# Optimization experiments

Measured on AMD Instinct MI355X. Metric: run time of the kernel, lower is better.

## Reference

```python
import jax, jax.numpy as jnp
import numpy as np

N, M, D = 8192, 8192, 1024

def setup_inputs() -> dict:
    key = jax.random.key(0)
    k1, k2 = jax.random.split(key)
    encoder_outputs = jax.random.normal(k1, (N, D), dtype=jnp.float32)
    fact_emb = jax.random.normal(k2, (M, D), dtype=jnp.float32)
    return {"encoder_outputs": encoder_outputs, "fact_emb": fact_emb}

def reference(encoder_outputs, fact_emb):
    # energy: [N, M] = encoder_outputs @ fact_emb^T (unscaled)
    energy = jnp.einsum('nd,md->nm', encoder_outputs, fact_emb)
    weights = jax.nn.softmax(energy, axis=1)          # softmax over facts
    outputs = jnp.einsum('nm,md->nd', weights, fact_emb)
    return (outputs, weights)
```

## Files before the change

kernel.cpp:

```cpp
#include <hip/hip_runtime.h>
#include <hip/hip_bf16.h>
#include <math.h>
#include <stdint.h>

#define N_ROWS 8192
#define M_FACTS 8192
#define D_DIM 1024

typedef __bf16 bf16x8_t __attribute__((ext_vector_type(8)));
typedef __bf16 bf16x4_t __attribute__((ext_vector_type(4)));
typedef float f32x4_t __attribute__((ext_vector_type(4)));

#define BM 128
#define BN 128
#define BK 32
#define PADK 40

__device__ __forceinline__ void gload_lds16(const void* g, void* lds) {
  __builtin_amdgcn_global_load_lds(
      (__attribute__((address_space(1))) void*)(uintptr_t)g,
      (__attribute__((address_space(3))) void*)(uint32_t)(uintptr_t)lds,
      16, 0, 0);
}


__global__ __launch_bounds__(256) void split_hi_lo(const float* __restrict__ X,
                                                   __bf16* __restrict__ H,
                                                   __bf16* __restrict__ L) {
  int i = blockIdx.x * 256 + threadIdx.x;
  float4 v = ((const float4*)X)[i];
  float f[4] = {v.x, v.y, v.z, v.w};
  bf16x4_t h, l;
#pragma unroll
  for (int q = 0; q < 4; q++) {
    __bf16 hh = (__bf16)f[q];
    h[q] = hh;
    l[q] = (__bf16)(f[q] - (float)hh);
  }
  ((bf16x4_t*)H)[i] = h;
  ((bf16x4_t*)L)[i] = l;
}

__global__ __launch_bounds__(256) void transpose_f_bf16(const float* __restrict__ F,
                                                        __bf16* __restrict__ Ft) {
  __shared__ __bf16 t[64 * 68];
  const int tid = threadIdx.x;
  const int m0 = blockIdx.x * 64, d0 = blockIdx.y * 64;
#pragma unroll
  for (int p = 0; p < 4; p++) {
    int flat = p * 256 + tid;
    int m = flat >> 4, dq = flat & 15;
    float4 v = *(const float4*)(F + (size_t)(m0 + m) * D_DIM + d0 + dq * 4);
    bf16x4_t h;
    h[0] = (__bf16)v.x;
    h[1] = (__bf16)v.y;
    h[2] = (__bf16)v.z;
    h[3] = (__bf16)v.w;
    *(bf16x4_t*)(t + m * 68 + dq * 4) = h;
  }
  __syncthreads();
  int d = tid & 63, mc = (tid >> 6) * 16;
  bf16x8_t o0, o1;
#pragma unroll
  for (int j = 0; j < 8; j++) o0[j] = t[(mc + j) * 68 + d];
#pragma unroll
  for (int j = 0; j < 8; j++) o1[j] = t[(mc + 8 + j) * 68 + d];
  __bf16* dst = Ft + (size_t)(d0 + d) * M_FACTS + m0 + mc;
  *(bf16x8_t*)(dst) = o0;
  *(bf16x8_t*)(dst + 8) = o1;
}

__global__ __launch_bounds__(256) void gemm1_fast(const __bf16* __restrict__ Eh,
                                                  const __bf16* __restrict__ El,
                                                  const __bf16* __restrict__ Fh,
                                                  const __bf16* __restrict__ Fl,
                                                  float* __restrict__ C) {
  __shared__ __bf16 sAh[BM * BK], sAl[BM * BK], sBh[BN * BK], sBl[BN * BK];
  const int tid = threadIdx.x;
  const int wave = tid >> 6, lane = tid & 63;
  const int row0 = blockIdx.x * BM, col0 = blockIdx.y * BN;
  const int wm = wave >> 1, wn = wave & 1;
  const int lrow = lane & 15, quad = lane >> 4;

  f32x4_t acc[4][4];
#pragma unroll
  for (int i = 0; i < 4; i++)
#pragma unroll
    for (int j = 0; j < 4; j++) acc[i][j] = (f32x4_t){0.f, 0.f, 0.f, 0.f};

  for (int k0 = 0; k0 < D_DIM; k0 += BK) {
#pragma unroll
    for (int r = 0; r < 2; r++) {
      int c = (r * 4 + wave) * 64 + lane;
      int row = c >> 2;
      int ko = (c & 3) << 3;
      size_t ga = (size_t)(row0 + row) * D_DIM + k0 + ko;
      size_t gb = (size_t)(col0 + row) * D_DIM + k0 + ko;
      gload_lds16(Eh + ga, sAh + c * 8);
      gload_lds16(El + ga, sAl + c * 8);
      gload_lds16(Fh + gb, sBh + c * 8);
      gload_lds16(Fl + gb, sBl + c * 8);
    }
    __syncthreads();

    bf16x8_t ah[4], al[4], bh[4], bl[4];
#pragma unroll
    for (int i = 0; i < 4; i++) {
      int ra = (wm * 64 + i * 16 + lrow) * BK + quad * 8;
      ah[i] = *(const bf16x8_t*)(sAh + ra);
      al[i] = *(const bf16x8_t*)(sAl + ra);
      int rb = (wn * 64 + i * 16 + lrow) * BK + quad * 8;
      bh[i] = *(const bf16x8_t*)(sBh + rb);
      bl[i] = *(const bf16x8_t*)(sBl + rb);
    }
#pragma unroll
    for (int i = 0; i < 4; i++)
#pragma unroll
      for (int j = 0; j < 4; j++) {
        acc[i][j] = __builtin_amdgcn_mfma_f32_16x16x32_bf16(ah[i], bh[j], acc[i][j], 0, 0, 0);
        acc[i][j] = __builtin_amdgcn_mfma_f32_16x16x32_bf16(ah[i], bl[j], acc[i][j], 0, 0, 0);
        acc[i][j] = __builtin_amdgcn_mfma_f32_16x16x32_bf16(al[i], bh[j], acc[i][j], 0, 0, 0);
      }
    __syncthreads();
  }

#pragma unroll
  for (int i = 0; i < 4; i++) {
    int rbase = row0 + wm * 64 + i * 16 + quad * 4;
#pragma unroll
    for (int j = 0; j < 4; j++) {
      int c = col0 + wn * 64 + j * 16 + lrow;
#pragma unroll
      for (int r = 0; r < 4; r++) C[(size_t)(rbase + r) * M_FACTS + c] = acc[i][j][r];
    }
  }
}

__global__ __launch_bounds__(256) void gemm2_fast(const __bf16* __restrict__ Wb,
                                                  const __bf16* __restrict__ Ft,
                                                  float* __restrict__ O,
                                                  int out_row0) {
  __shared__ __bf16 sW[BM * BK], sF[BN * BK];
  const int tid = threadIdx.x;
  const int wave = tid >> 6, lane = tid & 63;
  const int row0 = blockIdx.x * BM, col0 = blockIdx.y * BN;
  const int wm = wave >> 1, wn = wave & 1;
  const int lrow = lane & 15, quad = lane >> 4;

  f32x4_t acc[4][4];
#pragma unroll
  for (int i = 0; i < 4; i++)
#pragma unroll
    for (int j = 0; j < 4; j++) acc[i][j] = (f32x4_t){0.f, 0.f, 0.f, 0.f};

  for (int k0 = 0; k0 < M_FACTS; k0 += BK) {
#pragma unroll
    for (int r = 0; r < 2; r++) {
      int c = (r * 4 + wave) * 64 + lane;
      int row = c >> 2;
      int ko = (c & 3) << 3;
      gload_lds16(Wb + (size_t)(row0 + row) * M_FACTS + k0 + ko, sW + c * 8);
      gload_lds16(Ft + (size_t)(col0 + row) * M_FACTS + k0 + ko, sF + c * 8);
    }
    __syncthreads();

    bf16x8_t a[4], b[4];
#pragma unroll
    for (int i = 0; i < 4; i++) {
      a[i] = *(const bf16x8_t*)(sW + (wm * 64 + i * 16 + lrow) * BK + quad * 8);
      b[i] = *(const bf16x8_t*)(sF + (wn * 64 + i * 16 + lrow) * BK + quad * 8);
    }
#pragma unroll
    for (int i = 0; i < 4; i++)
#pragma unroll
      for (int j = 0; j < 4; j++)
        acc[i][j] = __builtin_amdgcn_mfma_f32_16x16x32_bf16(a[i], b[j], acc[i][j], 0, 0, 0);
    __syncthreads();
  }

#pragma unroll
  for (int i = 0; i < 4; i++) {
    int rbase = out_row0 + row0 + wm * 64 + i * 16 + quad * 4;
#pragma unroll
    for (int j = 0; j < 4; j++) {
      int c = col0 + wn * 64 + j * 16 + lrow;
#pragma unroll
      for (int r = 0; r < 4; r++) O[(size_t)(rbase + r) * D_DIM + c] = acc[i][j][r];
    }
  }
}

__global__ __launch_bounds__(256) void gemm2_mid(const float* __restrict__ W,
                                                 const __bf16* __restrict__ Ft,
                                                 float* __restrict__ O) {
  __shared__ __bf16 sW[BM * BK], sF[BN * BK];
  const int tid = threadIdx.x;
  const int wave = tid >> 6, lane = tid & 63;
  const int row0 = blockIdx.x * BM, col0 = blockIdx.y * BN;
  const int wm = wave >> 1, wn = wave & 1;
  const int lrow = lane & 15, quad = lane >> 4;

  f32x4_t acc[4][4];
#pragma unroll
  for (int i = 0; i < 4; i++)
#pragma unroll
    for (int j = 0; j < 4; j++) acc[i][j] = (f32x4_t){0.f, 0.f, 0.f, 0.f};

  for (int k0 = 0; k0 < M_FACTS; k0 += BK) {
#pragma unroll
    for (int r = 0; r < 2; r++) {
      int c = (r * 4 + wave) * 64 + lane;
      int row = c >> 2;
      int ko = (c & 3) << 3;
      gload_lds16(Ft + (size_t)(col0 + row) * M_FACTS + k0 + ko, sF + c * 8);
    }
#pragma unroll
    for (int it = 0; it < 4; it++) {
      int flat = it * 256 + tid;
      int r = flat >> 3, q = flat & 7;
      float4 v = *(const float4*)(W + (size_t)(row0 + r) * M_FACTS + k0 + q * 4);
      bf16x4_t h;
      h[0] = (__bf16)v.x;
      h[1] = (__bf16)v.y;
      h[2] = (__bf16)v.z;
      h[3] = (__bf16)v.w;
      *(bf16x4_t*)(sW + r * BK + q * 4) = h;
    }
    __syncthreads();

    bf16x8_t a[4], b[4];
#pragma unroll
    for (int i = 0; i < 4; i++) {
      a[i] = *(const bf16x8_t*)(sW + (wm * 64 + i * 16 + lrow) * BK + quad * 8);
      b[i] = *(const bf16x8_t*)(sF + (wn * 64 + i * 16 + lrow) * BK + quad * 8);
    }
#pragma unroll
    for (int i = 0; i < 4; i++)
#pragma unroll
      for (int j = 0; j < 4; j++)
        acc[i][j] = __builtin_amdgcn_mfma_f32_16x16x32_bf16(a[i], b[j], acc[i][j], 0, 0, 0);
    __syncthreads();
  }

#pragma unroll
  for (int i = 0; i < 4; i++) {
    int rbase = row0 + wm * 64 + i * 16 + quad * 4;
#pragma unroll
    for (int j = 0; j < 4; j++) {
      int c = col0 + wn * 64 + j * 16 + lrow;
#pragma unroll
      for (int r = 0; r < 4; r++) O[(size_t)(rbase + r) * D_DIM + c] = acc[i][j][r];
    }
  }
}

template <bool EMIT_BF16>
__global__ __launch_bounds__(256) void softmax_rows_t(float* __restrict__ W,
                                                      __bf16* __restrict__ Wb) {
  __shared__ float red[8];
  const int tid = threadIdx.x;
  float* p = W + (size_t)blockIdx.x * M_FACTS;

  float4 v[8];
  float mx = -3.4e38f;
#pragma unroll
  for (int i = 0; i < 8; i++) {
    v[i] = *(const float4*)(p + (size_t)(i * 256 + tid) * 4);
    mx = fmaxf(mx, fmaxf(fmaxf(v[i].x, v[i].y), fmaxf(v[i].z, v[i].w)));
  }
#pragma unroll
  for (int off = 32; off >= 1; off >>= 1) mx = fmaxf(mx, __shfl_xor(mx, off));
  const int wave = tid >> 6, lane = tid & 63;
  if (lane == 0) red[wave] = mx;
  __syncthreads();
  mx = fmaxf(fmaxf(red[0], red[1]), fmaxf(red[2], red[3]));

  float s = 0.f;
#pragma unroll
  for (int i = 0; i < 8; i++) {
    v[i].x = __expf(v[i].x - mx);
    v[i].y = __expf(v[i].y - mx);
    v[i].z = __expf(v[i].z - mx);
    v[i].w = __expf(v[i].w - mx);
    s += v[i].x + v[i].y + v[i].z + v[i].w;
  }
#pragma unroll
  for (int off = 32; off >= 1; off >>= 1) s += __shfl_xor(s, off);
  if (lane == 0) red[4 + wave] = s;
  __syncthreads();
  s = red[4] + red[5] + red[6] + red[7];
  float inv = 1.0f / s;
  __bf16* pb = EMIT_BF16 ? (Wb + (size_t)blockIdx.x * M_FACTS) : nullptr;
#pragma unroll
  for (int i = 0; i < 8; i++) {
    v[i].x *= inv;
    v[i].y *= inv;
    v[i].z *= inv;
    v[i].w *= inv;
    *(float4*)(p + (size_t)(i * 256 + tid) * 4) = v[i];
    if (EMIT_BF16) {
      bf16x4_t h;
      h[0] = (__bf16)v[i].x;
      h[1] = (__bf16)v[i].y;
      h[2] = (__bf16)v[i].z;
      h[3] = (__bf16)v[i].w;
      *(bf16x4_t*)(pb + (size_t)(i * 256 + tid) * 4) = h;
    }
  }
}

__global__ __launch_bounds__(256) void gemm1_energy(const float* __restrict__ A,
                                                    const float* __restrict__ B,
                                                    float* __restrict__ C) {
  __shared__ __align__(16) __bf16 sAh[BM * PADK];
  __shared__ __align__(16) __bf16 sAl[BM * PADK];
  __shared__ __align__(16) __bf16 sBh[BN * PADK];
  __shared__ __align__(16) __bf16 sBl[BN * PADK];

  const int tid = threadIdx.x;
  const int row0 = blockIdx.x * BM, col0 = blockIdx.y * BN;
  const int wave = tid >> 6, lane = tid & 63;
  const int wm = wave >> 1, wn = wave & 1;
  const int lrow = lane & 15, quad = lane >> 4;

  f32x4_t acc[4][4];
#pragma unroll
  for (int i = 0; i < 4; i++)
#pragma unroll
    for (int j = 0; j < 4; j++) acc[i][j] = (f32x4_t){0.f, 0.f, 0.f, 0.f};

  for (int k0 = 0; k0 < D_DIM; k0 += BK) {
    __syncthreads();
#pragma unroll
    for (int it = 0; it < 4; it++) {
      int flat = it * 256 + tid;
      int r = flat >> 3, kq = flat & 7;
      float4 va = *(const float4*)(A + (size_t)(row0 + r) * D_DIM + k0 + kq * 4);
      float4 vb = *(const float4*)(B + (size_t)(col0 + r) * D_DIM + k0 + kq * 4);
      float fa[4] = {va.x, va.y, va.z, va.w};
      float fb[4] = {vb.x, vb.y, vb.z, vb.w};
      bf16x4_t ah, al, bh, bl;
#pragma unroll
      for (int q = 0; q < 4; q++) {
        __bf16 h = (__bf16)fa[q];
        ah[q] = h;
        al[q] = (__bf16)(fa[q] - (float)h);
        __bf16 g = (__bf16)fb[q];
        bh[q] = g;
        bl[q] = (__bf16)(fb[q] - (float)g);
      }
      *(bf16x4_t*)(sAh + r * PADK + kq * 4) = ah;
      *(bf16x4_t*)(sAl + r * PADK + kq * 4) = al;
      *(bf16x4_t*)(sBh + r * PADK + kq * 4) = bh;
      *(bf16x4_t*)(sBl + r * PADK + kq * 4) = bl;
    }
    __syncthreads();

    bf16x8_t a_h[4], a_l[4], b_h[4], b_l[4];
#pragma unroll
    for (int i = 0; i < 4; i++) {
      int ra = wm * 64 + i * 16 + lrow;
      a_h[i] = *(const bf16x8_t*)(sAh + ra * PADK + quad * 8);
      a_l[i] = *(const bf16x8_t*)(sAl + ra * PADK + quad * 8);
      int rb = wn * 64 + i * 16 + lrow;
      b_h[i] = *(const bf16x8_t*)(sBh + rb * PADK + quad * 8);
      b_l[i] = *(const bf16x8_t*)(sBl + rb * PADK + quad * 8);
    }
#pragma unroll
    for (int i = 0; i < 4; i++)
#pragma unroll
      for (int j = 0; j < 4; j++) {
        acc[i][j] = __builtin_amdgcn_mfma_f32_16x16x32_bf16(a_h[i], b_h[j], acc[i][j], 0, 0, 0);
        acc[i][j] = __builtin_amdgcn_mfma_f32_16x16x32_bf16(a_h[i], b_l[j], acc[i][j], 0, 0, 0);
        acc[i][j] = __builtin_amdgcn_mfma_f32_16x16x32_bf16(a_l[i], b_h[j], acc[i][j], 0, 0, 0);
      }
  }

#pragma unroll
  for (int i = 0; i < 4; i++) {
    int rbase = row0 + wm * 64 + i * 16 + quad * 4;
#pragma unroll
    for (int j = 0; j < 4; j++) {
      int c = col0 + wn * 64 + j * 16 + lrow;
#pragma unroll
      for (int r = 0; r < 4; r++) C[(size_t)(rbase + r) * M_FACTS + c] = acc[i][j][r];
    }
  }
}

__global__ __launch_bounds__(256) void gemm2_out(const float* __restrict__ W,
                                                 const float* __restrict__ F,
                                                 float* __restrict__ O) {
  __shared__ __align__(16) __bf16 sW[BM * PADK];
  __shared__ __align__(16) __bf16 sFt[BN * PADK];

  const int tid = threadIdx.x;
  const int row0 = blockIdx.x * BM, col0 = blockIdx.y * BN;
  const int wave = tid >> 6, lane = tid & 63;
  const int wm = wave >> 1, wn = wave & 1;
  const int lrow = lane & 15, quad = lane >> 4;

  f32x4_t acc[4][4];
#pragma unroll
  for (int i = 0; i < 4; i++)
#pragma unroll
    for (int j = 0; j < 4; j++) acc[i][j] = (f32x4_t){0.f, 0.f, 0.f, 0.f};

  for (int k0 = 0; k0 < M_FACTS; k0 += BK) {
    __syncthreads();
#pragma unroll
    for (int it = 0; it < 4; it++) {
      int flat = it * 256 + tid;
      int r = flat >> 3, kq = flat & 7;
      float4 v = *(const float4*)(W + (size_t)(row0 + r) * M_FACTS + k0 + kq * 4);
      bf16x4_t h;
      h[0] = (__bf16)v.x;
      h[1] = (__bf16)v.y;
      h[2] = (__bf16)v.z;
      h[3] = (__bf16)v.w;
      *(bf16x4_t*)(sW + r * PADK + kq * 4) = h;
    }
#pragma unroll
    for (int it = 0; it < 4; it++) {
      int flat = it * 256 + tid;
      int m = flat >> 5, dq = flat & 31;
      float4 v = *(const float4*)(F + (size_t)(k0 + m) * D_DIM + col0 + dq * 4);
      sFt[(dq * 4 + 0) * PADK + m] = (__bf16)v.x;
      sFt[(dq * 4 + 1) * PADK + m] = (__bf16)v.y;
      sFt[(dq * 4 + 2) * PADK + m] = (__bf16)v.z;
      sFt[(dq * 4 + 3) * PADK + m] = (__bf16)v.w;
    }
    __syncthreads();

    bf16x8_t a[4], b[4];
#pragma unroll
    for (int i = 0; i < 4; i++) {
      a[i] = *(const bf16x8_t*)(sW + (wm * 64 + i * 16 + lrow) * PADK + quad * 8);
      b[i] = *(const bf16x8_t*)(sFt + (wn * 64 + i * 16 + lrow) * PADK + quad * 8);
    }
#pragma unroll
    for (int i = 0; i < 4; i++)
#pragma unroll
      for (int j = 0; j < 4; j++)
        acc[i][j] = __builtin_amdgcn_mfma_f32_16x16x32_bf16(a[i], b[j], acc[i][j], 0, 0, 0);
  }

#pragma unroll
  for (int i = 0; i < 4; i++) {
    int rbase = row0 + wm * 64 + i * 16 + quad * 4;
#pragma unroll
    for (int j = 0; j < 4; j++) {
      int c = col0 + wn * 64 + j * 16 + lrow;
#pragma unroll
      for (int r = 0; r < 4; r++) O[(size_t)(rbase + r) * D_DIM + c] = acc[i][j][r];
    }
  }
}

extern "C" void kernel_launch(void* const* d_in, const int* in_sizes, int n_in,
                              void* d_out, int out_size, void* d_ws, size_t ws_size,
                              hipStream_t stream) {
  const float* E = (const float*)d_in[0];
  const float* F = (const float*)d_in[1];
  float* outputs = (float*)d_out;
  float* weights = (float*)d_out + (size_t)N_ROWS * D_DIM;

  const size_t MB = 1ull << 20;
  char* ws = (char*)d_ws;

  const bool t1 = ws_size >= 144 * MB;
  const bool t2 = !t1 && ws_size >= 80 * MB;
  const bool hasFtOnly = !t1 && !t2 && ws_size >= 16 * MB;

  if (t1) {
    __bf16* Eh = (__bf16*)(ws + 0 * MB);
    __bf16* El = (__bf16*)(ws + 16 * MB);
    __bf16* Fh = (__bf16*)(ws + 32 * MB);
    __bf16* Fl = (__bf16*)(ws + 48 * MB);
    __bf16* Wb = (__bf16*)(ws + 0 * MB);
    __bf16* Ft = (__bf16*)(ws + 128 * MB);

    transpose_f_bf16<<<dim3(M_FACTS / 64, D_DIM / 64), 256, 0, stream>>>(F, Ft);
    split_hi_lo<<<dim3((N_ROWS * D_DIM) / 1024), 256, 0, stream>>>(E, Eh, El);
    split_hi_lo<<<dim3((M_FACTS * D_DIM) / 1024), 256, 0, stream>>>(F, Fh, Fl);
    gemm1_fast<<<dim3(N_ROWS / BM, M_FACTS / BN), 256, 0, stream>>>(Eh, El, Fh, Fl, weights);
    softmax_rows_t<true><<<dim3(N_ROWS), 256, 0, stream>>>(weights, Wb);
    gemm2_fast<<<dim3(N_ROWS / BM, D_DIM / BN), 256, 0, stream>>>(Wb, Ft, outputs, 0);
  } else if (t2) {
    __bf16* Eh = (__bf16*)(ws + 0 * MB);
    __bf16* El = (__bf16*)(ws + 16 * MB);
    __bf16* Fh = (__bf16*)(ws + 32 * MB);
    __bf16* Fl = (__bf16*)(ws + 48 * MB);
    __bf16* Wb = (__bf16*)(ws + 0 * MB);
    __bf16* Ft = (__bf16*)(ws + 64 * MB);

    transpose_f_bf16<<<dim3(M_FACTS / 64, D_DIM / 64), 256, 0, stream>>>(F, Ft);
    split_hi_lo<<<dim3((N_ROWS * D_DIM) / 1024), 256, 0, stream>>>(E, Eh, El);
    split_hi_lo<<<dim3((M_FACTS * D_DIM) / 1024), 256, 0, stream>>>(F, Fh, Fl);
    gemm1_fast<<<dim3(N_ROWS / BM, M_FACTS / BN), 256, 0, stream>>>(Eh, El, Fh, Fl, weights);

    const int HALF = N_ROWS / 2;
    for (int h = 0; h < 2; h++) {
      float* Wchunk = weights + (size_t)h * HALF * M_FACTS;
      softmax_rows_t<true><<<dim3(HALF), 256, 0, stream>>>(Wchunk, Wb);
      gemm2_fast<<<dim3(HALF / BM, D_DIM / BN), 256, 0, stream>>>(Wb, Ft, outputs, h * HALF);
    }
  } else {
    __bf16* Ft = (__bf16*)ws;
    if (hasFtOnly) {
      transpose_f_bf16<<<dim3(M_FACTS / 64, D_DIM / 64), 256, 0, stream>>>(F, Ft);
    }
    gemm1_energy<<<dim3(N_ROWS / BM, M_FACTS / BN), 256, 0, stream>>>(E, F, weights);
    softmax_rows_t<false><<<dim3(N_ROWS), 256, 0, stream>>>(weights, nullptr);
    if (hasFtOnly) {
      gemm2_mid<<<dim3(N_ROWS / BM, D_DIM / BN), 256, 0, stream>>>(weights, Ft, outputs);
    } else {
      gemm2_out<<<dim3(N_ROWS / BM, D_DIM / BN), 256, 0, stream>>>(weights, F, outputs);
    }
  }
}
```

Before: 1.012 ms.

## Double-buffer gemm2 LDS loads with BK=64 and swap grid order

```diff
diff --git a/kernel.cpp b/kernel.cpp
--- a/kernel.cpp
+++ b/kernel.cpp
@@ -22,6 +22,8 @@
       (__attribute__((address_space(3))) void*)(uint32_t)(uintptr_t)lds,
       16, 0, 0);
 }
+
+#define WAIT_VMCNT(n) __builtin_amdgcn_s_waitcnt(0x0F70 | (n))
 
 
 __global__ __launch_bounds__(256) void split_hi_lo(const float* __restrict__ X,
@@ -136,46 +138,73 @@
   }
 }
 
-__global__ __launch_bounds__(256) void gemm2_fast(const __bf16* __restrict__ Wb,
-                                                  const __bf16* __restrict__ Ft,
-                                                  float* __restrict__ O,
-                                                  int out_row0) {
-  __shared__ __bf16 sW[BM * BK], sF[BN * BK];
+#define G2BK 64
+__global__ __launch_bounds__(256) void gemm2_db(const __bf16* __restrict__ Wb,
+                                                const __bf16* __restrict__ Ft,
+                                                float* __restrict__ O,
+                                                int out_row0) {
+  __shared__ __bf16 sW[2][BM * G2BK];
+  __shared__ __bf16 sF[2][BN * G2BK];
   const int tid = threadIdx.x;
   const int wave = tid >> 6, lane = tid & 63;
-  const int row0 = blockIdx.x * BM, col0 = blockIdx.y * BN;
+  const int col0 = blockIdx.x * BN;
+  const int row0 = blockIdx.y * BM;
   const int wm = wave >> 1, wn = wave & 1;
   const int lrow = lane & 15, quad = lane >> 4;
 
+  const int lr = lane >> 3;
+  const int lk = (lane & 7) * 8;
+
   f32x4_t acc[4][4];
 #pragma unroll
   for (int i = 0; i < 4; i++)
 #pragma unroll
     for (int j = 0; j < 4; j++) acc[i][j] = (f32x4_t){0.f, 0.f, 0.f, 0.f};
 
-  for (int k0 = 0; k0 < M_FACTS; k0 += BK) {
-#pragma unroll
-    for (int r = 0; r < 2; r++) {
-      int c = (r * 4 + wave) * 64 + lane;
-      int row = c >> 2;
-      int ko = (c & 3) << 3;
-      gload_lds16(Wb + (size_t)(row0 + row) * M_FACTS + k0 + ko, sW + c * 8);
-      gload_lds16(Ft + (size_t)(col0 + row) * M_FACTS + k0 + ko, sF + c * 8);
-    }
-    __syncthreads();
-
-    bf16x8_t a[4], b[4];
-#pragma unroll
-    for (int i = 0; i < 4; i++) {
-      a[i] = *(const bf16x8_t*)(sW + (wm * 64 + i * 16 + lrow) * BK + quad * 8);
-      b[i] = *(const bf16x8_t*)(sF + (wn * 64 + i * 16 + lrow) * BK + quad * 8);
-    }
-#pragma unroll
-    for (int i = 0; i < 4; i++)
-#pragma unroll
-      for (int j = 0; j < 4; j++)
-        acc[i][j] = __builtin_amdgcn_mfma_f32_16x16x32_bf16(a[i], b[j], acc[i][j], 0, 0, 0);
-    __syncthreads();
+#pragma unroll
+  for (int r = 0; r < 4; r++) {
+    int c = wave * 4 + r;
+    int row = c * 8 + lr;
+    gload_lds16(Wb + (size_t)(row0 + row) * M_FACTS + 0 + lk, &sW[0][c * 512 + lane * 8]);
+    gload_lds16(Ft + (size_t)(col0 + row) * M_FACTS + 0 + lk, &sF[0][c * 512 + lane * 8]);
+  }
+
+  int buf = 0;
+  for (int k0 = 0; k0 < M_FACTS; k0 += G2BK) {
+    const bool more = (k0 + G2BK) < M_FACTS;
+    if (more) {
+      int nb = buf ^ 1;
+#pragma unroll
+      for (int r = 0; r < 4; r++) {
+        int c = wave * 4 + r;
+        int row = c * 8 + lr;
+        gload_lds16(Wb + (size_t)(row0 + row) * M_FACTS + (k0 + G2BK) + lk,
+                    &sW[nb][c * 512 + lane * 8]);
+        gload_lds16(Ft + (size_t)(col0 + row) * M_FACTS + (k0 + G2BK) + lk,
+                    &sF[nb][c * 512 + lane * 8]);
+      }
+      WAIT_VMCNT(8);
+    } else {
+      WAIT_VMCNT(0);
+    }
+    __builtin_amdgcn_s_barrier();
+
+#pragma unroll
+    for (int ks = 0; ks < G2BK; ks += 32) {
+      bf16x8_t a[4], b[4];
+#pragma unroll
+      for (int i = 0; i < 4; i++) {
+        a[i] = *(const bf16x8_t*)(&sW[buf][(wm * 64 + i * 16 + lrow) * G2BK + ks + quad * 8]);
+        b[i] = *(const bf16x8_t*)(&sF[buf][(wn * 64 + i * 16 + lrow) * G2BK + ks + quad * 8]);
+      }
+#pragma unroll
+      for (int i = 0; i < 4; i++)
+#pragma unroll
+        for (int j = 0; j < 4; j++)
+          acc[i][j] = __builtin_amdgcn_mfma_f32_16x16x32_bf16(a[i], b[j], acc[i][j], 0, 0, 0);
+    }
+    __builtin_amdgcn_s_barrier();
+    buf ^= 1;
   }
 
 #pragma unroll
@@ -472,38 +501,29 @@
   const bool t2 = !t1 && ws_size >= 80 * MB;
   const bool hasFtOnly = !t1 && !t2 && ws_size >= 16 * MB;
 
-  if (t1) {
-    __bf16* Eh = (__bf16*)(ws + 0 * MB);
-    __bf16* El = (__bf16*)(ws + 16 * MB);
-    __bf16* Fh = (__bf16*)(ws + 32 * MB);
-    __bf16* Fl = (__bf16*)(ws + 48 * MB);
-    __bf16* Wb = (__bf16*)(ws + 0 * MB);
-    __bf16* Ft = (__bf16*)(ws + 128 * MB);
+  if (t1 || t2) {
+    __bf16* Ft = (__bf16*)(ws + 0 * MB);
+    __bf16* Eh = (__bf16*)(ws + 16 * MB);
+    __bf16* El = (__bf16*)(ws + 32 * MB);
+    __bf16* Fh = (__bf16*)(ws + 48 * MB);
+    __bf16* Fl = (__bf16*)(ws + 64 * MB);
+    __bf16* Wb = (__bf16*)(ws + 16 * MB);
 
     transpose_f_bf16<<<dim3(M_FACTS / 64, D_DIM / 64), 256, 0, stream>>>(F, Ft);
     split_hi_lo<<<dim3((N_ROWS * D_DIM) / 1024), 256, 0, stream>>>(E, Eh, El);
     split_hi_lo<<<dim3((M_FACTS * D_DIM) / 1024), 256, 0, stream>>>(F, Fh, Fl);
     gemm1_fast<<<dim3(N_ROWS / BM, M_FACTS / BN), 256, 0, stream>>>(Eh, El, Fh, Fl, weights);
-    softmax_rows_t<true><<<dim3(N_ROWS), 256, 0, stream>>>(weights, Wb);
-    gemm2_fast<<<dim3(N_ROWS / BM, D_DIM / BN), 256, 0, stream>>>(Wb, Ft, outputs, 0);
-  } else if (t2) {
-    __bf16* Eh = (__bf16*)(ws + 0 * MB);
-    __bf16* El = (__bf16*)(ws + 16 * MB);
-    __bf16* Fh = (__bf16*)(ws + 32 * MB);
-    __bf16* Fl = (__bf16*)(ws + 48 * MB);
-    __bf16* Wb = (__bf16*)(ws + 0 * MB);
-    __bf16* Ft = (__bf16*)(ws + 64 * MB);
-
-    transpose_f_bf16<<<dim3(M_FACTS / 64, D_DIM / 64), 256, 0, stream>>>(F, Ft);
-    split_hi_lo<<<dim3((N_ROWS * D_DIM) / 1024), 256, 0, stream>>>(E, Eh, El);
-    split_hi_lo<<<dim3((M_FACTS * D_DIM) / 1024), 256, 0, stream>>>(F, Fh, Fl);
-    gemm1_fast<<<dim3(N_ROWS / BM, M_FACTS / BN), 256, 0, stream>>>(Eh, El, Fh, Fl, weights);
-
-    const int HALF = N_ROWS / 2;
-    for (int h = 0; h < 2; h++) {
-      float* Wchunk = weights + (size_t)h * HALF * M_FACTS;
-      softmax_rows_t<true><<<dim3(HALF), 256, 0, stream>>>(Wchunk, Wb);
-      gemm2_fast<<<dim3(HALF / BM, D_DIM / BN), 256, 0, stream>>>(Wb, Ft, outputs, h * HALF);
+
+    if (t1) {
+      softmax_rows_t<true><<<dim3(N_ROWS), 256, 0, stream>>>(weights, Wb);
+      gemm2_db<<<dim3(D_DIM / BN, N_ROWS / BM), 256, 0, stream>>>(Wb, Ft, outputs, 0);
+    } else {
+      const int HALF = N_ROWS / 2;
+      for (int h = 0; h < 2; h++) {
+        float* Wchunk = weights + (size_t)h * HALF * M_FACTS;
+        softmax_rows_t<true><<<dim3(HALF), 256, 0, stream>>>(Wchunk, Wb);
+        gemm2_db<<<dim3(D_DIM / BN, HALF / BM), 256, 0, stream>>>(Wb, Ft, outputs, h * HALF);
+      }
     }
   } else {
     __bf16* Ft = (__bf16*)ws;
```

After: 998.8 us. No clear change (-1.3%).
